# Kernel optimization log

Hardware: AMD Instinct MI355X
Metric: run time of the kernel (lower is better)

## Reference

```python
import jax, jax.numpy as jnp
import numpy as np


def setup_inputs() -> dict:
    key = jax.random.key(0)
    k1, k2 = jax.random.split(key)
    B, D, C = 4096, 128, 64
    score = jax.random.normal(k1, (B, D), dtype=jnp.float32)
    target = jax.random.randint(k2, (B,), 0, C, dtype=jnp.int64)
    alpha = jnp.full((1,), 9.0, dtype=jnp.float32)  # learned margin param
    return {"score": score, "target": target, "alpha": alpha}


def _pairwise_dist(score):
    # squared euclidean: ||xi||^2 + ||xj||^2 - 2 xi.xj, clamped at 0, then sqrt
    mag = jnp.sum(score * score, axis=1)            # [B]
    d2 = mag[:, None] + mag[None, :] - 2.0 * (score @ score.T)
    d2 = jnp.maximum(d2, 0.0)
    # safe sqrt (diagonal is exactly 0; avoid nan grads)
    safe = jnp.where(d2 > 0.0, d2, 1.0)
    return jnp.where(d2 > 0.0, jnp.sqrt(safe), 0.0)  # [B, B]


def reference(score, target, alpha):
    target = target.reshape(-1)
    B = score.shape[0]
    dist = _pairwise_dist(score)                    # [B, B]
    diff = target[:, None] != target[None, :]       # [B, B] negative-pair mask
    # per-anchor sum over negatives of exp(alpha - dist); diagonal excluded (same label)
    nes = jnp.sum(jnp.where(diff, jnp.exp(alpha[0] - dist), 0.0), axis=1)  # [B]
    l_n = jnp.log(nes[:, None] + nes[None, :])      # [B, B]
    # positive pairs i<j with equal labels
    upper = jnp.triu(jnp.ones((B, B), dtype=bool), k=1)
    pos = (~diff) & upper
    terms = jnp.where(pos, jax.nn.relu(l_n + dist) ** 2, 0.0)
    counter = jnp.sum(pos).astype(score.dtype)
    return jnp.sum(terms) / (2.0 * counter)
```

## Files before the change

kernel.cpp:

```cpp
#include <hip/hip_runtime.h>
#include <math.h>

#define BN 4096
#define DD 128
#define NWT 64
#define NTILES (NWT * (NWT + 1) / 2)
#define NJB 64
#define SLOTS 1024
#define OVCAP (4u * 1024u * 1024u)

typedef __attribute__((ext_vector_type(8))) short short8;
typedef __attribute__((ext_vector_type(4))) float f32x4;

__device__ __forceinline__ unsigned short f2bf(float f) {
    unsigned int u = __float_as_uint(f);
    u += 0x7FFFu + ((u >> 16) & 1u);
    return (unsigned short)(u >> 16);
}


__global__ __launch_bounds__(256)
void prep_kernel(const float* __restrict__ score, unsigned short* __restrict__ sbf,
                 float* __restrict__ mag) {
    int row  = blockIdx.x * 4 + (threadIdx.x >> 6);
    int lane = threadIdx.x & 63;
    float2 v = *reinterpret_cast<const float2*>(score + (size_t)row * DD + lane * 2);
    float s = v.x * v.x + v.y * v.y;
    #pragma unroll
    for (int off = 32; off; off >>= 1) s += __shfl_xor(s, off);
    ushort2 u; u.x = f2bf(v.x); u.y = f2bf(v.y);
    *reinterpret_cast<ushort2*>(sbf + (size_t)row * DD + lane * 2) = u;
    if (lane == 0) mag[row] = s;
}

__global__ __launch_bounds__(256)
void nes_kernel(const unsigned short* __restrict__ sbf, const int* __restrict__ target,
                const float* __restrict__ alphap, const float* __restrict__ mag,
                float* __restrict__ nes_part,
                uint2* __restrict__ recs, uint2* __restrict__ ovrecs,
                int* __restrict__ tilecnt, unsigned int* __restrict__ ovcnt) {
    const int tid = threadIdx.x;
    const int w = tid >> 6, lane = tid & 63;
    const int lhi = lane >> 4, llo = lane & 15;
    const int t = blockIdx.x * 4 + w;
    if (t >= NTILES) return;

    int ib = 0, rem = t, rl = NWT;
    while (rem >= rl) { rem -= rl; ++ib; --rl; }
    const int jb = ib + rem;
    const int i0 = ib * 64, j0 = jb * 64;
    const bool diag = (ib == jb);

    short8 a[4][4], b[4][4];
    #pragma unroll
    for (int m = 0; m < 4; ++m)
        #pragma unroll
        for (int kk = 0; kk < 4; ++kk)
            a[m][kk] = *reinterpret_cast<const short8*>(
                sbf + (size_t)(i0 + m * 16 + llo) * DD + kk * 32 + lhi * 8);
    #pragma unroll
    for (int n = 0; n < 4; ++n)
        #pragma unroll
        for (int kk = 0; kk < 4; ++kk)
            b[n][kk] = *reinterpret_cast<const short8*>(
                sbf + (size_t)(j0 + n * 16 + llo) * DD + kk * 32 + lhi * 8);

    f32x4 acc[4][4] = {};
    #pragma unroll
    for (int kk = 0; kk < 4; ++kk)
        #pragma unroll
        for (int m = 0; m < 4; ++m)
            #pragma unroll
            for (int n = 0; n < 4; ++n)
                acc[m][n] = __builtin_amdgcn_mfma_f32_16x16x32_bf16(a[m][kk], b[n][kk], acc[m][n], 0, 0, 0);

    const float alpha = alphap[0];
    float mj[4]; int tj[4]; int jj[4];
    #pragma unroll
    for (int n = 0; n < 4; ++n) {
        int j = j0 + n * 16 + llo;
        jj[n] = j; mj[n] = mag[j]; tj[n] = target[j];
    }
    float cs[4] = {0.f, 0.f, 0.f, 0.f};
    unsigned int wbase = 0;
    #pragma unroll
    for (int m = 0; m < 4; ++m) {
        #pragma unroll
        for (int rg = 0; rg < 4; ++rg) {
            int i = i0 + m * 16 + lhi * 4 + rg;
            float mi = mag[i];
            int ti = target[i];
            float rs = 0.f;
            #pragma unroll
            for (int n = 0; n < 4; ++n) {
                float d2 = fmaxf(mi + mj[n] - 2.0f * acc[m][n][rg], 0.0f);
                float dist = sqrtf(d2);
                bool p = (ti == tj[n]);
                float e = p ? 0.0f : __expf(alpha - dist);
                rs += e;
                cs[n] += e;
                bool emit = p && (jj[n] > i);
                unsigned long long mask = __ballot(emit);
                if (emit) {
                    unsigned pos = (unsigned)__popcll(mask & ((1ULL << lane) - 1ULL));
                    unsigned slot = wbase + pos;
                    uint2 r;
                    r.x = __float_as_uint(dist);
                    r.y = ((unsigned)i << 16) | (unsigned)jj[n];
                    if (slot < SLOTS) recs[(size_t)t * SLOTS + slot] = r;
                    else {
                        unsigned o = atomicAdd(ovcnt, 1u);
                        if (o < OVCAP) ovrecs[o] = r;
                    }
                }
                wbase += (unsigned)__popcll(mask);
            }
            rs += __shfl_xor(rs, 1);
            rs += __shfl_xor(rs, 2);
            rs += __shfl_xor(rs, 4);
            rs += __shfl_xor(rs, 8);
            if (llo == 0) nes_part[(size_t)jb * BN + i] = rs;
        }
    }
    #pragma unroll
    for (int n = 0; n < 4; ++n) {
        cs[n] += __shfl_xor(cs[n], 16);
        cs[n] += __shfl_xor(cs[n], 32);
        if (!diag && lane < 16)
            nes_part[(size_t)ib * BN + jj[n]] = cs[n];
    }
    if (lane == 0) tilecnt[t] = (int)wbase;
}

__global__ __launch_bounds__(256)
void nes_reduce_kernel(const float* __restrict__ nes_part, float* __restrict__ nes) {
    int t = blockIdx.x * 256 + threadIdx.x;
    float s = 0.f;
    #pragma unroll
    for (int k = 0; k < NJB; ++k) s += nes_part[(size_t)k * BN + t];
    nes[t] = s;
}

__global__ __launch_bounds__(256)
void pos_kernel(const uint2* __restrict__ recs, const uint2* __restrict__ ovrecs,
                const int* __restrict__ tilecnt, const unsigned int* __restrict__ ovcnt,
                const float* __restrict__ nes,
                float* __restrict__ part_sum, unsigned int* __restrict__ part_cnt) {
    __shared__ float ssum[4];
    __shared__ unsigned int scnt[4];
    const int t = blockIdx.x;
    const int tid = threadIdx.x;
    const int w = tid >> 6;
    int cnt = tilecnt[t];
    if (cnt > SLOTS) cnt = SLOTS;
    float s = 0.f;
    unsigned int cc = 0;
    for (int k = tid; k < cnt; k += 256) {
        uint2 r = recs[(size_t)t * SLOTS + k];
        float dist = __uint_as_float(r.x);
        int i = r.y >> 16, j = r.y & 0xFFFF;
        float tv = __logf(nes[i] + nes[j]) + dist;
        if (tv > 0.f) s += tv * tv;
        cc++;
    }
    unsigned int oc = *ovcnt;
    if (oc > OVCAP) oc = OVCAP;
    for (unsigned int k = (unsigned)t * 256u + tid; k < oc; k += (unsigned)NTILES * 256u) {
        uint2 r = ovrecs[k];
        float dist = __uint_as_float(r.x);
        int i = r.y >> 16, j = r.y & 0xFFFF;
        float tv = __logf(nes[i] + nes[j]) + dist;
        if (tv > 0.f) s += tv * tv;
        cc++;
    }
    #pragma unroll
    for (int off = 1; off < 64; off <<= 1) {
        s += __shfl_xor(s, off);
        cc += __shfl_xor(cc, off);
    }
    if ((tid & 63) == 0) { ssum[w] = s; scnt[w] = cc; }
    __syncthreads();
    if (tid == 0) {
        part_sum[t] = ssum[0] + ssum[1] + ssum[2] + ssum[3];
        part_cnt[t] = scnt[0] + scnt[1] + scnt[2] + scnt[3];
    }
}

__global__ __launch_bounds__(256)
void finalize_kernel(const float* __restrict__ part_sum,
                     const unsigned int* __restrict__ part_cnt,
                     float* __restrict__ out) {
    __shared__ float fs[4];
    __shared__ unsigned int fc[4];
    int tid = threadIdx.x;
    float s = 0.f;
    unsigned int c = 0;
    #pragma unroll
    for (int k = 0; k < 9; ++k) {
        int idx = k * 256 + tid;
        if (idx < NTILES) {
            s += part_sum[idx];
            c += part_cnt[idx];
        }
    }
    #pragma unroll
    for (int off = 1; off < 64; off <<= 1) {
        s += __shfl_xor(s, off);
        c += __shfl_xor(c, off);
    }
    if ((tid & 63) == 0) { fs[tid >> 6] = s; fc[tid >> 6] = c; }
    __syncthreads();
    if (tid == 0) {
        float S = fs[0] + fs[1] + fs[2] + fs[3];
        float C = (float)(fc[0] + fc[1] + fc[2] + fc[3]);
        out[0] = S / (2.0f * C);
    }
}

extern "C" void kernel_launch(void* const* d_in, const int* in_sizes, int n_in,
                              void* d_out, int out_size, void* d_ws, size_t ws_size,
                              hipStream_t stream) {
    const float* score  = (const float*)d_in[0];
    const int*   target = (const int*)d_in[1];
    const float* alpha  = (const float*)d_in[2];
    float* out = (float*)d_out;

    unsigned short* sbf = (unsigned short*)d_ws;
    float* mag      = (float*)((char*)d_ws + (size_t)BN * DD * 2);
    float* nes_part = mag + BN;
    float* nes      = nes_part + (size_t)NJB * BN;
    float* part_sum = nes + BN;
    unsigned int* part_cnt = (unsigned int*)(part_sum + NTILES);
    int* tilecnt    = (int*)(part_cnt + NTILES);
    unsigned int* ovcnt = (unsigned int*)(tilecnt + NTILES);
    uint2* recs     = (uint2*)(ovcnt + 16);
    uint2* ovrecs   = recs + (size_t)NTILES * SLOTS;

    hipMemsetAsync(ovcnt, 0, sizeof(unsigned int), stream);

    prep_kernel<<<BN / 4, 256, 0, stream>>>(score, sbf, mag);
    nes_kernel<<<(NTILES + 3) / 4, 256, 0, stream>>>(sbf, target, alpha, mag, nes_part,
                                                     recs, ovrecs, tilecnt, ovcnt);
    nes_reduce_kernel<<<BN / 256, 256, 0, stream>>>(nes_part, nes);
    pos_kernel<<<NTILES, 256, 0, stream>>>(recs, ovrecs, tilecnt, ovcnt, nes,
                                           part_sum, part_cnt);
    finalize_kernel<<<1, 256, 0, stream>>>(part_sum, part_cnt, out);
}
```

Before: 127.3 us.

## Split each 64x64 tile into four 32x32 wave quadrants, one block per tile

Each block now handles one 64x64 upper-triangle tile, and each of its four waves computes a 32x32 quadrant instead of a whole tile. This gives four times as many wavefronts with fewer accumulators per wave, aiming for more parallelism and occupancy across CUs in the MFMA/exp stage. The per-quadrant record slots, the nes partial buffer (now 128 strips) and the pos kernel indexing are adjusted to match. The cost is redundant A/B operand loads across waves and a reduction twice as wide in nes_reduce.

```diff
diff --git a/kernel.cpp b/kernel.cpp
--- a/kernel.cpp
+++ b/kernel.cpp
@@ -5,8 +5,9 @@
 #define DD 128
 #define NWT 64
 #define NTILES (NWT * (NWT + 1) / 2)
-#define NJB 64
-#define SLOTS 1024
+#define NQ (NTILES * 4)
+#define NJB2 128
+#define QSLOTS 512
 #define OVCAP (4u * 1024u * 1024u)
 
 typedef __attribute__((ext_vector_type(8))) short short8;
@@ -42,49 +43,50 @@
     const int tid = threadIdx.x;
     const int w = tid >> 6, lane = tid & 63;
     const int lhi = lane >> 4, llo = lane & 15;
-    const int t = blockIdx.x * 4 + w;
-    if (t >= NTILES) return;
+    const int t = blockIdx.x;
+    const int qr = w >> 1, qc = w & 1;
+    const int qid = t * 4 + w;
 
     int ib = 0, rem = t, rl = NWT;
     while (rem >= rl) { rem -= rl; ++ib; --rl; }
     const int jb = ib + rem;
-    const int i0 = ib * 64, j0 = jb * 64;
+    const int i0 = ib * 64 + qr * 32, j0 = jb * 64 + qc * 32;
     const bool diag = (ib == jb);
 
-    short8 a[4][4], b[4][4];
-    #pragma unroll
-    for (int m = 0; m < 4; ++m)
+    short8 a[2][4], b[2][4];
+    #pragma unroll
+    for (int m = 0; m < 2; ++m)
         #pragma unroll
         for (int kk = 0; kk < 4; ++kk)
             a[m][kk] = *reinterpret_cast<const short8*>(
                 sbf + (size_t)(i0 + m * 16 + llo) * DD + kk * 32 + lhi * 8);
     #pragma unroll
-    for (int n = 0; n < 4; ++n)
+    for (int n = 0; n < 2; ++n)
         #pragma unroll
         for (int kk = 0; kk < 4; ++kk)
             b[n][kk] = *reinterpret_cast<const short8*>(
                 sbf + (size_t)(j0 + n * 16 + llo) * DD + kk * 32 + lhi * 8);
 
-    f32x4 acc[4][4] = {};
+    f32x4 acc[2][2] = {};
     #pragma unroll
     for (int kk = 0; kk < 4; ++kk)
         #pragma unroll
-        for (int m = 0; m < 4; ++m)
+        for (int m = 0; m < 2; ++m)
             #pragma unroll
-            for (int n = 0; n < 4; ++n)
+            for (int n = 0; n < 2; ++n)
                 acc[m][n] = __builtin_amdgcn_mfma_f32_16x16x32_bf16(a[m][kk], b[n][kk], acc[m][n], 0, 0, 0);
 
     const float alpha = alphap[0];
-    float mj[4]; int tj[4]; int jj[4];
-    #pragma unroll
-    for (int n = 0; n < 4; ++n) {
+    float mj[2]; int tj[2]; int jj[2];
+    #pragma unroll
+    for (int n = 0; n < 2; ++n) {
         int j = j0 + n * 16 + llo;
         jj[n] = j; mj[n] = mag[j]; tj[n] = target[j];
     }
-    float cs[4] = {0.f, 0.f, 0.f, 0.f};
+    float cs[2] = {0.f, 0.f};
     unsigned int wbase = 0;
     #pragma unroll
-    for (int m = 0; m < 4; ++m) {
+    for (int m = 0; m < 2; ++m) {
         #pragma unroll
         for (int rg = 0; rg < 4; ++rg) {
             int i = i0 + m * 16 + lhi * 4 + rg;
@@ -92,7 +94,7 @@
             int ti = target[i];
             float rs = 0.f;
             #pragma unroll
-            for (int n = 0; n < 4; ++n) {
+            for (int n = 0; n < 2; ++n) {
                 float d2 = fmaxf(mi + mj[n] - 2.0f * acc[m][n][rg], 0.0f);
                 float dist = sqrtf(d2);
                 bool p = (ti == tj[n]);
@@ -107,7 +109,7 @@
                     uint2 r;
                     r.x = __float_as_uint(dist);
                     r.y = ((unsigned)i << 16) | (unsigned)jj[n];
-                    if (slot < SLOTS) recs[(size_t)t * SLOTS + slot] = r;
+                    if (slot < QSLOTS) recs[(size_t)qid * QSLOTS + slot] = r;
                     else {
                         unsigned o = atomicAdd(ovcnt, 1u);
                         if (o < OVCAP) ovrecs[o] = r;
@@ -119,17 +121,17 @@
             rs += __shfl_xor(rs, 2);
             rs += __shfl_xor(rs, 4);
             rs += __shfl_xor(rs, 8);
-            if (llo == 0) nes_part[(size_t)jb * BN + i] = rs;
+            if (llo == 0) nes_part[(size_t)(jb * 2 + qc) * BN + i] = rs;
         }
     }
     #pragma unroll
-    for (int n = 0; n < 4; ++n) {
+    for (int n = 0; n < 2; ++n) {
         cs[n] += __shfl_xor(cs[n], 16);
         cs[n] += __shfl_xor(cs[n], 32);
         if (!diag && lane < 16)
-            nes_part[(size_t)ib * BN + jj[n]] = cs[n];
-    }
-    if (lane == 0) tilecnt[t] = (int)wbase;
+            nes_part[(size_t)(ib * 2 + qr) * BN + jj[n]] = cs[n];
+    }
+    if (lane == 0) tilecnt[qid] = (int)wbase;
 }
 
 __global__ __launch_bounds__(256)
@@ -137,7 +139,7 @@
     int t = blockIdx.x * 256 + threadIdx.x;
     float s = 0.f;
     #pragma unroll
-    for (int k = 0; k < NJB; ++k) s += nes_part[(size_t)k * BN + t];
+    for (int k = 0; k < NJB2; ++k) s += nes_part[(size_t)k * BN + t];
     nes[t] = s;
 }
 
@@ -148,24 +150,28 @@
                 float* __restrict__ part_sum, unsigned int* __restrict__ part_cnt) {
     __shared__ float ssum[4];
     __shared__ unsigned int scnt[4];
-    const int t = blockIdx.x;
+    const int bidx = blockIdx.x;
     const int tid = threadIdx.x;
     const int w = tid >> 6;
-    int cnt = tilecnt[t];
-    if (cnt > SLOTS) cnt = SLOTS;
     float s = 0.f;
     unsigned int cc = 0;
-    for (int k = tid; k < cnt; k += 256) {
-        uint2 r = recs[(size_t)t * SLOTS + k];
-        float dist = __uint_as_float(r.x);
-        int i = r.y >> 16, j = r.y & 0xFFFF;
-        float tv = __logf(nes[i] + nes[j]) + dist;
-        if (tv > 0.f) s += tv * tv;
-        cc++;
+    #pragma unroll
+    for (int qq = 0; qq < 4; ++qq) {
+        int qid = bidx * 4 + qq;
+        int cnt = tilecnt[qid];
+        if (cnt > QSLOTS) cnt = QSLOTS;
+        for (int k = tid; k < cnt; k += 256) {
+            uint2 r = recs[(size_t)qid * QSLOTS + k];
+            float dist = __uint_as_float(r.x);
+            int i = r.y >> 16, j = r.y & 0xFFFF;
+            float tv = __logf(nes[i] + nes[j]) + dist;
+            if (tv > 0.f) s += tv * tv;
+            cc++;
+        }
     }
     unsigned int oc = *ovcnt;
     if (oc > OVCAP) oc = OVCAP;
-    for (unsigned int k = (unsigned)t * 256u + tid; k < oc; k += (unsigned)NTILES * 256u) {
+    for (unsigned int k = (unsigned)bidx * 256u + tid; k < oc; k += (unsigned)NTILES * 256u) {
         uint2 r = ovrecs[k];
         float dist = __uint_as_float(r.x);
         int i = r.y >> 16, j = r.y & 0xFFFF;
@@ -181,8 +187,8 @@
     if ((tid & 63) == 0) { ssum[w] = s; scnt[w] = cc; }
     __syncthreads();
     if (tid == 0) {
-        part_sum[t] = ssum[0] + ssum[1] + ssum[2] + ssum[3];
-        part_cnt[t] = scnt[0] + scnt[1] + scnt[2] + scnt[3];
+        part_sum[bidx] = ssum[0] + ssum[1] + ssum[2] + ssum[3];
+        part_cnt[bidx] = scnt[0] + scnt[1] + scnt[2] + scnt[3];
     }
 }
 
@@ -228,19 +234,19 @@
     unsigned short* sbf = (unsigned short*)d_ws;
     float* mag      = (float*)((char*)d_ws + (size_t)BN * DD * 2);
     float* nes_part = mag + BN;
-    float* nes      = nes_part + (size_t)NJB * BN;
+    float* nes      = nes_part + (size_t)NJB2 * BN;
     float* part_sum = nes + BN;
     unsigned int* part_cnt = (unsigned int*)(part_sum + NTILES);
     int* tilecnt    = (int*)(part_cnt + NTILES);
-    unsigned int* ovcnt = (unsigned int*)(tilecnt + NTILES);
+    unsigned int* ovcnt = (unsigned int*)(tilecnt + NQ);
     uint2* recs     = (uint2*)(ovcnt + 16);
-    uint2* ovrecs   = recs + (size_t)NTILES * SLOTS;
+    uint2* ovrecs   = recs + (size_t)NQ * QSLOTS;
 
     hipMemsetAsync(ovcnt, 0, sizeof(unsigned int), stream);
 
     prep_kernel<<<BN / 4, 256, 0, stream>>>(score, sbf, mag);
-    nes_kernel<<<(NTILES + 3) / 4, 256, 0, stream>>>(sbf, target, alpha, mag, nes_part,
-                                                     recs, ovrecs, tilecnt, ovcnt);
+    nes_kernel<<<NTILES, 256, 0, stream>>>(sbf, target, alpha, mag, nes_part,
+                                           recs, ovrecs, tilecnt, ovcnt);
     nes_reduce_kernel<<<BN / 256, 256, 0, stream>>>(nes_part, nes);
     pos_kernel<<<NTILES, 256, 0, stream>>>(recs, ovrecs, tilecnt, ovcnt, nes,
                                            part_sum, part_cnt);
```

Measured after the change: 131.8 us. 1.04x slower.
